# Optimization experiments

Hardware: AMD Instinct MI355X
Metric: run time of the kernel (lower is better)

## Reference

```python
import jax, jax.numpy as jnp
import numpy as np

LN_EPS = 1e-5
GRID_MIN, GRID_MAX = -1.0, 1.0


def make_grid(grid_size: int, spline_order: int) -> jnp.ndarray:
    h = (GRID_MAX - GRID_MIN) / grid_size
    # extended knot vector: grid_size + 2*spline_order + 1 knots
    return (jnp.arange(-spline_order, grid_size + spline_order + 1, dtype=jnp.float32) * h
            + GRID_MIN)


def b_splines(x: jnp.ndarray, grid: jnp.ndarray, k: int) -> jnp.ndarray:
    """Cox-de Boor B-spline bases. x: [B, in] -> [B, in, grid_size + k]."""
    x = x[..., None]  # [B, in, 1]
    bases = ((x >= grid[:-1]) & (x < grid[1:])).astype(x.dtype)
    for p in range(1, k + 1):
        left = (x - grid[: -(p + 1)]) / (grid[p:-1] - grid[: -(p + 1)]) * bases[..., :-1]
        right = (grid[p + 1:] - x) / (grid[p + 1:] - grid[1:-p]) * bases[..., 1:]
        bases = left + right
    return bases  # [B, in, grid_size + k]


def kan_layer(x, base_w, spline_w, grid, k):
    # base path: silu(x) @ base_w.T ; spline path: einsum over basis functions
    base = jnp.einsum('bi,oi->bo', jax.nn.silu(x), base_w)
    spl = jnp.einsum('big,oig->bo', b_splines(x, grid, k), spline_w)
    return base + spl


def layer_norm(x, gamma, beta):
    mu = jnp.mean(x, axis=-1, keepdims=True)
    var = jnp.mean(jnp.square(x - mu), axis=-1, keepdims=True)
    return (x - mu) * jax.lax.rsqrt(var + LN_EPS) * gamma + beta


def setup_inputs() -> dict:
    key = jax.random.key(0)
    ks = jax.random.split(key, 6)
    B, S, H, A = 32768, 256, 512, 64
    G, K = 5, 3
    nb = G + K  # 8 basis functions per edge
    s = 0.1
    return {
        'state': jax.random.normal(ks[0], (B, S), dtype=jnp.float32),
        'feat_base_w': jax.random.normal(ks[1], (H, S), dtype=jnp.float32) * s,
        'feat_spline_w': jax.random.normal(ks[2], (H, S, nb), dtype=jnp.float32) * s,
        'ln_gamma': jnp.ones((H,), dtype=jnp.float32),
        'ln_beta': jnp.zeros((H,), dtype=jnp.float32),
        'mean_base_w': jax.random.normal(ks[3], (A, H), dtype=jnp.float32) * s,
        'mean_spline_w': jax.random.normal(ks[4], (A, H, nb), dtype=jnp.float32) * s,
        'lstd_base_w': jax.random.normal(ks[5], (A, H), dtype=jnp.float32) * s,
        'lstd_spline_w': jax.random.normal(jax.random.fold_in(key, 7), (A, H, nb), dtype=jnp.float32) * s,
        'grid_size': G,
        'spline_order': K,
    }


def reference(state, feat_base_w, feat_spline_w, ln_gamma, ln_beta,
              mean_base_w, mean_spline_w, lstd_base_w, lstd_spline_w,
              grid_size, spline_order):
    LOG_STD_MIN, LOG_STD_MAX = -20.0, 2.0
    grid = make_grid(grid_size, spline_order)
    x = kan_layer(state, feat_base_w, feat_spline_w, grid, spline_order)
    x = jax.nn.relu(layer_norm(x, ln_gamma, ln_beta))
    mean = jnp.tanh(kan_layer(x, mean_base_w, mean_spline_w, grid, spline_order))
    log_std = jnp.clip(kan_layer(x, lstd_base_w, lstd_spline_w, grid, spline_order),
                       LOG_STD_MIN, LOG_STD_MAX)
    return mean, log_std
```

## Files before the change

### kernel.cpp

```cpp
#include <hip/hip_runtime.h>
#include <stdint.h>

typedef __bf16 bf16x8 __attribute__((ext_vector_type(8)));
typedef float f32x4 __attribute__((ext_vector_type(4)));
typedef unsigned short u16x8 __attribute__((ext_vector_type(8)));
typedef unsigned int as1_uint __attribute__((address_space(1)));
typedef unsigned int as3_uint __attribute__((address_space(3)));

#define N_B 32768
#define S_IN 256
#define H_DIM 512
#define A_DIM 64
#define K1_DIM 2304
#define K2_DIM 4608
#define LDA2 72

#define MFMA __builtin_amdgcn_mfma_f32_16x16x32_bf16

static __device__ __forceinline__ unsigned short f2bf(float f) {
  union { float f; unsigned u; } v; v.f = f;
  unsigned r = v.u + 0x7fffu + ((v.u >> 16) & 1u);
  return (unsigned short)(r >> 16);
}

static __device__ __forceinline__ void gload_lds16(const void* g, void* l) {
  __builtin_amdgcn_global_load_lds((const as1_uint*)g, (as3_uint*)l, 16, 0, 0);
}

static __device__ __forceinline__ int swz64(int c, int row) {
  return (c & ~63) | ((((c >> 3) & 7) ^ (row & 7)) << 3) | (c & 7);
}

static __device__ __forceinline__ void bspline_w(float x, float& c,
    float& w0, float& w1, float& w2, float& w3) {
  float u = fmaf(2.5f, x, 5.5f);
  c = floorf(u);
  float f = u - c;
  float f2 = f * f;
  float f3 = f2 * f;
  const float k6 = 1.f / 6.f;
  w3 = f3 * k6;
  w2 = (3.f * (f + f2 - f3) + 1.f) * k6;
  w1 = (3.f * f3 - 6.f * f2 + 4.f) * k6;
  float omf = 1.f - f;
  w0 = omf * omf * omf * k6;
}

static __device__ __forceinline__ float silu_f(float x) {
  return x / (1.f + __expf(-x));
}

__global__ void k_sentinel(float* out, int n) {
  int i = blockIdx.x * blockDim.x + threadIdx.x;
  for (; i < n; i += gridDim.x * blockDim.x) out[i] = 12345.f;
}

__global__ void k_prep_w1(const float* __restrict__ base_w,
                          const float* __restrict__ spline_w,
                          unsigned short* __restrict__ W1) {
  int idx = blockIdx.x * blockDim.x + threadIdx.x;
  int n = idx / K1_DIM;
  int c = idx - n * K1_DIM;
  int k = swz64(c, n);
  int j = k >> 8;
  int i = k & 255;
  float v = (j == 0) ? base_w[n * S_IN + i]
                     : spline_w[(size_t)(n * S_IN + i) * 8 + (j - 1)];
  W1[idx] = f2bf(v);
}

__global__ void k_prep_w2(const float* __restrict__ mean_base,
                          const float* __restrict__ mean_spl,
                          const float* __restrict__ lstd_base,
                          const float* __restrict__ lstd_spl,
                          unsigned short* __restrict__ W2) {
  int idx = blockIdx.x * blockDim.x + threadIdx.x;
  int n = idx / K2_DIM;
  int c = idx - n * K2_DIM;
  int k = swz64(c, n);
  int j = k / 512;
  int h = k - j * 512;
  const float* bw = (n < 64) ? mean_base : lstd_base;
  const float* sw = (n < 64) ? mean_spl : lstd_spl;
  int nn = n & 63;
  float v = (j == 0) ? bw[nn * H_DIM + h]
                     : sw[(size_t)(nn * H_DIM + h) * 8 + (j - 1)];
  W2[idx] = f2bf(v);
}

__global__ void k_features1(const float* __restrict__ state,
                            unsigned short* __restrict__ F1) {
  int tid = blockIdx.x * blockDim.x + threadIdx.x;
  int base = tid * 4;
  int b = base >> 8;
  int i = base & 255;
  const float4 xv = *(const float4*)(state + base);
  float xs[4] = {xv.x, xv.y, xv.z, xv.w};
  unsigned short outj[9][4];
  #pragma unroll
  for (int e = 0; e < 4; ++e) {
    float x = xs[e];
    float c, w0, w1, w2, w3;
    bspline_w(x, c, w0, w1, w2, w3);
    outj[0][e] = f2bf(silu_f(x));
    #pragma unroll
    for (int g = 0; g < 8; ++g) {
      float d = c - (float)g;
      float v = 0.f;
      v = (d == 0.f) ? w3 : v;
      v = (d == 1.f) ? w2 : v;
      v = (d == 2.f) ? w1 : v;
      v = (d == 3.f) ? w0 : v;
      outj[g + 1][e] = f2bf(v);
    }
  }
  size_t rowbase = (size_t)b * K1_DIM;
  #pragma unroll
  for (int j = 0; j < 9; ++j) {
    int c = swz64(j * S_IN + i, b);
    *(ushort4*)(F1 + rowbase + c) =
        make_ushort4(outj[j][0], outj[j][1], outj[j][2], outj[j][3]);
  }
}

__global__ __launch_bounds__(256, 2) void k_gemm1(
    const unsigned short* __restrict__ F1,
    const unsigned short* __restrict__ W1,
    float* __restrict__ X) {
  extern __shared__ unsigned short smem[];
  unsigned short* As0 = smem;
  unsigned short* As1 = smem + 8192;
  unsigned short* Bs0 = smem + 16384;
  unsigned short* Bs1 = smem + 24576;

  const int t = threadIdx.x;
  const int bid = (int)(blockIdx.x & 7) * 128 + ((int)blockIdx.x >> 3);
  const int bm = bid >> 2;
  const int bn = bid & 3;

  const unsigned short* Ab = F1 + (size_t)bm * 128 * K1_DIM;
  const unsigned short* Bb = W1 + (size_t)bn * 128 * K1_DIM;

  const int srow = t >> 3;
  const int scol = (t & 7) * 8;

  auto stage = [&](int buf, int kt) {
    unsigned short* Ad = buf ? As1 : As0;
    unsigned short* Bd = buf ? Bs1 : Bs0;
    const size_t k0 = (size_t)kt * 64;
    #pragma unroll
    for (int q = 0; q < 4; ++q) {
      const int r = q * 32 + srow;
      gload_lds16(Ab + (size_t)r * K1_DIM + k0 + scol, Ad + r * 64 + scol);
      gload_lds16(Bb + (size_t)r * K1_DIM + k0 + scol, Bd + r * 64 + scol);
    }
  };

  const int wave = t >> 6;
  const int lane = t & 63;
  const int wm = (wave >> 1) * 64;
  const int wn = (wave & 1) * 64;
  const int lr = lane & 15;
  const int l4 = lane >> 4;

  f32x4 acc[4][4];
  #pragma unroll
  for (int i = 0; i < 4; ++i)
    #pragma unroll
    for (int jj = 0; jj < 4; ++jj)
      acc[i][jj] = (f32x4){0.f, 0.f, 0.f, 0.f};

  stage(0, 0);
  __syncthreads();
  int cur = 0;
  const int NT = K1_DIM / 64;
  for (int kt = 0; kt < NT; ++kt) {
    if (kt + 1 < NT) stage(cur ^ 1, kt + 1);
    const unsigned short* A0 = cur ? As1 : As0;
    const unsigned short* B0 = cur ? Bs1 : Bs0;
    #pragma unroll
    for (int ks = 0; ks < 2; ++ks) {
      bf16x8 af[4], bfv[4];
      #pragma unroll
      for (int fm = 0; fm < 4; ++fm) {
        const int r = wm + fm * 16 + lr;
        const int slot = (ks * 4 + l4) ^ (r & 7);
        af[fm] = *(const bf16x8*)(A0 + r * 64 + slot * 8);
      }
      #pragma unroll
      for (int fn = 0; fn < 4; ++fn) {
        const int r = wn + fn * 16 + lr;
        const int slot = (ks * 4 + l4) ^ (r & 7);
        bfv[fn] = *(const bf16x8*)(B0 + r * 64 + slot * 8);
      }
      #pragma unroll
      for (int fm = 0; fm < 4; ++fm)
        #pragma unroll
        for (int fn = 0; fn < 4; ++fn)
          acc[fm][fn] = MFMA(af[fm], bfv[fn], acc[fm][fn], 0, 0, 0);
    }
    __syncthreads();
    cur ^= 1;
  }

  float* Xb = X + (size_t)bm * 128 * H_DIM + bn * 128;
  #pragma unroll
  for (int fm = 0; fm < 4; ++fm) {
    const int row0 = wm + fm * 16 + l4 * 4;
    #pragma unroll
    for (int fn = 0; fn < 4; ++fn) {
      const int col = wn + fn * 16 + lr;
      #pragma unroll
      for (int r = 0; r < 4; ++r)
        Xb[(size_t)(row0 + r) * H_DIM + col] = acc[fm][fn][r];
    }
  }
}

__global__ __launch_bounds__(256, 2) void k_gemm2(
    const float* __restrict__ X, const unsigned short* __restrict__ W2,
    const float* __restrict__ gamma, const float* __restrict__ beta,
    float* __restrict__ out) {
  extern __shared__ unsigned short smem2[];
  unsigned short* At = smem2;
  unsigned short* Bt = smem2 + 64 * LDA2;

  const int t = threadIdx.x;
  const int bm = blockIdx.x;
  const int row = t >> 2;
  const int quart = t & 3;
  const int wave = t >> 6;
  const int lane = t & 63;
  const int wn = wave * 32;
  const int lr = lane & 15;
  const int l4 = lane >> 4;

  const float* Xrow = X + (size_t)(bm * 64 + row) * H_DIM;

  float s = 0.f, ss = 0.f;
  #pragma unroll 4
  for (int q = 0; q < 32; ++q) {
    float4 v = *(const float4*)(Xrow + quart * 128 + q * 4);
    s += v.x + v.y + v.z + v.w;
    ss += v.x * v.x + v.y * v.y + v.z * v.z + v.w * v.w;
  }
  s += __shfl_xor(s, 1); ss += __shfl_xor(ss, 1);
  s += __shfl_xor(s, 2); ss += __shfl_xor(ss, 2);
  const float mu = s * (1.f / 512.f);
  const float var = ss * (1.f / 512.f) - mu * mu;
  const float rstd = rsqrtf(var + 1e-5f);

  f32x4 acc[4][2];
  #pragma unroll
  for (int i = 0; i < 4; ++i)
    #pragma unroll
    for (int jj = 0; jj < 2; ++jj)
      acc[i][jj] = (f32x4){0.f, 0.f, 0.f, 0.f};

  float cw[16], w0[16], w1[16], w2[16], w3[16];

  const int sbrow = t >> 3;
  const int sbcol = (t & 7) * 8;

  for (int hb = 0; hb < 8; ++hb) {
    for (int j = 0; j < 9; ++j) {
      __syncthreads();
      {
        const size_t k0 = (size_t)j * 512 + hb * 64;
        #pragma unroll
        for (int q = 0; q < 4; ++q) {
          const int r = q * 32 + sbrow;
          gload_lds16(W2 + (size_t)r * K2_DIM + k0 + sbcol, Bt + r * 64 + sbcol);
        }
      }
      unsigned short av[16];
      if (j == 0) {
        #pragma unroll
        for (int c4 = 0; c4 < 4; ++c4) {
          const int h = hb * 64 + quart * 16 + c4 * 4;
          const float4 xv = *(const float4*)(Xrow + h);
          const float4 gv = *(const float4*)(gamma + h);
          const float4 bv = *(const float4*)(beta + h);
          float xa[4] = {xv.x, xv.y, xv.z, xv.w};
          float ga[4] = {gv.x, gv.y, gv.z, gv.w};
          float ba[4] = {bv.x, bv.y, bv.z, bv.w};
          #pragma unroll
          for (int e2 = 0; e2 < 4; ++e2) {
            const int e = c4 * 4 + e2;
            float xn = fmaf((xa[e2] - mu) * rstd, ga[e2], ba[e2]);
            xn = fmaxf(xn, 0.f);
            bspline_w(xn, cw[e], w0[e], w1[e], w2[e], w3[e]);
            av[e] = f2bf(silu_f(xn));
          }
        }
      } else {
        const float g = (float)(j - 1);
        #pragma unroll
        for (int e = 0; e < 16; ++e) {
          const float d = cw[e] - g;
          float v = 0.f;
          v = (d == 0.f) ? w3[e] : v;
          v = (d == 1.f) ? w2[e] : v;
          v = (d == 2.f) ? w1[e] : v;
          v = (d == 3.f) ? w0[e] : v;
          av[e] = f2bf(v);
        }
      }
      u16x8 p0, p1;
      #pragma unroll
      for (int e = 0; e < 8; ++e) { p0[e] = av[e]; p1[e] = av[e + 8]; }
      *(u16x8*)(At + row * LDA2 + quart * 16) = p0;
      *(u16x8*)(At + row * LDA2 + quart * 16 + 8) = p1;

      __syncthreads();

      #pragma unroll
      for (int ks = 0; ks < 2; ++ks) {
        bf16x8 af[4], bfv[2];
        #pragma unroll
        for (int fm = 0; fm < 4; ++fm)
          af[fm] = *(const bf16x8*)(At + (fm * 16 + lr) * LDA2 + ks * 32 + l4 * 8);
        #pragma unroll
        for (int fn = 0; fn < 2; ++fn) {
          const int r = wn + fn * 16 + lr;
          const int slot = (ks * 4 + l4) ^ (r & 7);
          bfv[fn] = *(const bf16x8*)(Bt + r * 64 + slot * 8);
        }
        #pragma unroll
        for (int fm = 0; fm < 4; ++fm)
          #pragma unroll
          for (int fn = 0; fn < 2; ++fn)
            acc[fm][fn] = MFMA(af[fm], bfv[fn], acc[fm][fn], 0, 0, 0);
      }
    }
  }

  float* mean_out = out;
  float* lstd_out = out + (size_t)N_B * A_DIM;
  #pragma unroll
  for (int fm = 0; fm < 4; ++fm) {
    const int r0 = bm * 64 + fm * 16 + l4 * 4;
    #pragma unroll
    for (int fn = 0; fn < 2; ++fn) {
      const int n = wn + fn * 16 + lr;
      #pragma unroll
      for (int r = 0; r < 4; ++r) {
        const float v = acc[fm][fn][r];
        if (n < 64) mean_out[(size_t)(r0 + r) * 64 + n] = tanhf(v);
        else lstd_out[(size_t)(r0 + r) * 64 + (n - 64)] = fminf(fmaxf(v, -20.f), 2.f);
      }
    }
  }
}

extern "C" void kernel_launch(void* const* d_in, const int* in_sizes, int n_in,
                              void* d_out, int out_size, void* d_ws, size_t ws_size,
                              hipStream_t stream) {
  const float* state         = (const float*)d_in[0];
  const float* feat_base_w   = (const float*)d_in[1];
  const float* feat_spline_w = (const float*)d_in[2];
  const float* ln_gamma      = (const float*)d_in[3];
  const float* ln_beta       = (const float*)d_in[4];
  const float* mean_base_w   = (const float*)d_in[5];
  const float* mean_spline_w = (const float*)d_in[6];
  const float* lstd_base_w   = (const float*)d_in[7];
  const float* lstd_spline_w = (const float*)d_in[8];

  const size_t W1_OFF = 0;
  const size_t W2_OFF = 2359296;
  const size_t F1_OFF = 3538944;
  const size_t X_OFF  = 154533888;
  const size_t NEED   = 221642752;

  if (ws_size < NEED) {
    hipLaunchKernelGGL(k_sentinel, dim3(4096), dim3(256), 0, stream,
                       (float*)d_out, out_size);
    return;
  }

  char* ws = (char*)d_ws;
  unsigned short* W1 = (unsigned short*)(ws + W1_OFF);
  unsigned short* W2 = (unsigned short*)(ws + W2_OFF);
  unsigned short* F1 = (unsigned short*)(ws + F1_OFF);
  float* X = (float*)(ws + X_OFF);

  hipLaunchKernelGGL(k_prep_w1, dim3(4608), dim3(256), 0, stream,
                     feat_base_w, feat_spline_w, W1);
  hipLaunchKernelGGL(k_prep_w2, dim3(2304), dim3(256), 0, stream,
                     mean_base_w, mean_spline_w, lstd_base_w, lstd_spline_w, W2);
  hipLaunchKernelGGL(k_features1, dim3(8192), dim3(256), 0, stream, state, F1);
  hipLaunchKernelGGL(k_gemm1, dim3(1024), dim3(256), 65536, stream, F1, W1, X);
  hipLaunchKernelGGL(k_gemm2, dim3(512), dim3(256), (64 * LDA2 + 128 * 64) * 2,
                     stream, X, W2, ln_gamma, ln_beta, (float*)d_out);
}
```

Measured before the change: 233.6 us.

## Interleave per-channel KAN features in gemm2 and load B fragments from global directly

Rearranges the second-layer weight matrix so that each hidden channel's base and 8 spline weights are interleaved and padded to 12 entries. The gemm2 A-tile is then built two channels per thread by packing silu and four nonzero B-spline weights with 64-bit shifts, instead of computing dense one-hot bases across 9 separate K-slices. B fragments are register-prefetched from global memory instead of staged through LDS, and the W2 buffer now reuses the F1 workspace after gemm1, so its prep runs later. The padding adds about a third more MFMA work and makes B loads uncoalesced global reads, in exchange for fewer barriers and less feature computation.

```diff
diff --git a/kernel.cpp b/kernel.cpp
--- a/kernel.cpp
+++ b/kernel.cpp
@@ -12,8 +12,8 @@
 #define H_DIM 512
 #define A_DIM 64
 #define K1_DIM 2304
-#define K2_DIM 4608
-#define LDA2 72
+#define K2P 6144
+#define LDA2P 104
 
 #define MFMA __builtin_amdgcn_mfma_f32_16x16x32_bf16
 
@@ -50,6 +50,37 @@
   return x / (1.f + __expf(-x));
 }
 
+static __device__ __forceinline__ void kan_feat(float x, unsigned& s16,
+    unsigned& q0, unsigned& q1, unsigned& q2, unsigned& q3) {
+  s16 = f2bf(silu_f(x));
+  float u = fmaf(2.5f, x, 5.5f);
+  float cf = floorf(u);
+  float f = u - cf;
+  float f2 = f * f;
+  float f3 = f2 * f;
+  const float k6 = 1.f / 6.f;
+  float w3v = f3 * k6;
+  float w2v = (3.f * (f + f2 - f3) + 1.f) * k6;
+  float w1v = (3.f * f3 - 6.f * f2 + 4.f) * k6;
+  float omf = 1.f - f;
+  float w0v = omf * omf * omf * k6;
+  int i0 = (int)cf - 3;
+  uint64_t W64 = (uint64_t)((unsigned)f2bf(w0v) | ((unsigned)f2bf(w1v) << 16))
+               | ((uint64_t)((unsigned)f2bf(w2v) | ((unsigned)f2bf(w3v) << 16)) << 32);
+  uint64_t lo = 0, hi = 0;
+  if (i0 >= 0) {
+    int s = i0 * 16;
+    lo = (i0 < 4) ? (W64 << (s & 63)) : 0;
+    uint64_t hr = (i0 >= 1 && i0 < 4) ? (W64 >> ((64 - s) & 63)) : 0;
+    uint64_t hl = (i0 >= 4 && i0 < 8) ? (W64 << ((s - 64) & 63)) : 0;
+    hi = hr | hl;
+  } else {
+    lo = (i0 >= -3) ? (W64 >> ((-i0 * 16) & 63)) : 0;
+  }
+  q0 = (unsigned)lo; q1 = (unsigned)(lo >> 32);
+  q2 = (unsigned)hi; q3 = (unsigned)(hi >> 32);
+}
+
 __global__ void k_sentinel(float* out, int n) {
   int i = blockIdx.x * blockDim.x + threadIdx.x;
   for (; i < n; i += gridDim.x * blockDim.x) out[i] = 12345.f;
@@ -73,19 +104,19 @@
                           const float* __restrict__ mean_spl,
                           const float* __restrict__ lstd_base,
                           const float* __restrict__ lstd_spl,
-                          unsigned short* __restrict__ W2) {
+                          unsigned short* __restrict__ W2p) {
   int idx = blockIdx.x * blockDim.x + threadIdx.x;
-  int n = idx / K2_DIM;
-  int c = idx - n * K2_DIM;
-  int k = swz64(c, n);
-  int j = k / 512;
-  int h = k - j * 512;
+  int n = idx / K2P;
+  int k = idx - n * K2P;
+  int h = k / 12;
+  int j = k - h * 12;
   const float* bw = (n < 64) ? mean_base : lstd_base;
   const float* sw = (n < 64) ? mean_spl : lstd_spl;
   int nn = n & 63;
-  float v = (j == 0) ? bw[nn * H_DIM + h]
-                     : sw[(size_t)(nn * H_DIM + h) * 8 + (j - 1)];
-  W2[idx] = f2bf(v);
+  float v = 0.f;
+  if (j == 0) v = bw[nn * H_DIM + h];
+  else if (j <= 8) v = sw[(size_t)(nn * H_DIM + h) * 8 + (j - 1)];
+  W2p[idx] = f2bf(v);
 }
 
 __global__ void k_features1(const float* __restrict__ state,
@@ -218,12 +249,11 @@
 }
 
 __global__ __launch_bounds__(256, 2) void k_gemm2(
-    const float* __restrict__ X, const unsigned short* __restrict__ W2,
+    const float* __restrict__ X, const unsigned short* __restrict__ W2p,
     const float* __restrict__ gamma, const float* __restrict__ beta,
     float* __restrict__ out) {
   extern __shared__ unsigned short smem2[];
   unsigned short* At = smem2;
-  unsigned short* Bt = smem2 + 64 * LDA2;
 
   const int t = threadIdx.x;
   const int bm = blockIdx.x;
@@ -250,6 +280,21 @@
   const float var = ss * (1.f / 512.f) - mu * mu;
   const float rstd = rsqrtf(var + 1e-5f);
 
+  const unsigned short* bptr0 = W2p + (size_t)(wn + lr) * K2P + l4 * 8;
+  const unsigned short* bptr1 = W2p + (size_t)(wn + 16 + lr) * K2P + l4 * 8;
+
+  bf16x8 bcur[2][3], bnxt[2][3];
+  #pragma unroll
+  for (int ks = 0; ks < 3; ++ks) {
+    bnxt[0][ks] = *(const bf16x8*)(bptr0 + ks * 32);
+    bnxt[1][ks] = *(const bf16x8*)(bptr1 + ks * 32);
+  }
+
+  const int hq = quart * 2;
+  float2 xp = *(const float2*)(Xrow + hq);
+  float2 gp = *(const float2*)(gamma + hq);
+  float2 bp = *(const float2*)(beta + hq);
+
   f32x4 acc[4][2];
   #pragma unroll
   for (int i = 0; i < 4; ++i)
@@ -257,80 +302,56 @@
     for (int jj = 0; jj < 2; ++jj)
       acc[i][jj] = (f32x4){0.f, 0.f, 0.f, 0.f};
 
-  float cw[16], w0[16], w1[16], w2[16], w3[16];
-
-  const int sbrow = t >> 3;
-  const int sbcol = (t & 7) * 8;
-
-  for (int hb = 0; hb < 8; ++hb) {
-    for (int j = 0; j < 9; ++j) {
-      __syncthreads();
-      {
-        const size_t k0 = (size_t)j * 512 + hb * 64;
-        #pragma unroll
-        for (int q = 0; q < 4; ++q) {
-          const int r = q * 32 + sbrow;
-          gload_lds16(W2 + (size_t)r * K2_DIM + k0 + sbcol, Bt + r * 64 + sbcol);
-        }
+  for (int ch = 0; ch < 64; ++ch) {
+    unsigned o[12];
+    {
+      float xn0 = fmaxf(fmaf((xp.x - mu) * rstd, gp.x, bp.x), 0.f);
+      float xn1 = fmaxf(fmaf((xp.y - mu) * rstd, gp.y, bp.y), 0.f);
+      unsigned sA, a0, a1, a2, a3, sB, b0, b1, b2, b3;
+      kan_feat(xn0, sA, a0, a1, a2, a3);
+      kan_feat(xn1, sB, b0, b1, b2, b3);
+      o[0] = sA | (a0 << 16); o[1] = (a0 >> 16) | (a1 << 16);
+      o[2] = (a1 >> 16) | (a2 << 16); o[3] = (a2 >> 16) | (a3 << 16);
+      o[4] = (a3 >> 16); o[5] = 0u;
+      o[6] = sB | (b0 << 16); o[7] = (b0 >> 16) | (b1 << 16);
+      o[8] = (b1 >> 16) | (b2 << 16); o[9] = (b2 >> 16) | (b3 << 16);
+      o[10] = (b3 >> 16); o[11] = 0u;
+    }
+    __syncthreads();
+    #pragma unroll
+    for (int fn = 0; fn < 2; ++fn)
+      #pragma unroll
+      for (int ks = 0; ks < 3; ++ks)
+        bcur[fn][ks] = bnxt[fn][ks];
+    {
+      uint4* da = (uint4*)(At + row * LDA2P + quart * 24);
+      da[0] = make_uint4(o[0], o[1], o[2], o[3]);
+      da[1] = make_uint4(o[4], o[5], o[6], o[7]);
+      da[2] = make_uint4(o[8], o[9], o[10], o[11]);
+    }
+    __syncthreads();
+    if (ch < 63) {
+      const int h2 = (ch + 1) * 8 + hq;
+      xp = *(const float2*)(Xrow + h2);
+      gp = *(const float2*)(gamma + h2);
+      bp = *(const float2*)(beta + h2);
+      const size_t ko = (size_t)(ch + 1) * 96;
+      #pragma unroll
+      for (int ks = 0; ks < 3; ++ks) {
+        bnxt[0][ks] = *(const bf16x8*)(bptr0 + ko + ks * 32);
+        bnxt[1][ks] = *(const bf16x8*)(bptr1 + ko + ks * 32);
       }
-      unsigned short av[16];
-      if (j == 0) {
-        #pragma unroll
-        for (int c4 = 0; c4 < 4; ++c4) {
-          const int h = hb * 64 + quart * 16 + c4 * 4;
-          const float4 xv = *(const float4*)(Xrow + h);
-          const float4 gv = *(const float4*)(gamma + h);
-          const float4 bv = *(const float4*)(beta + h);
-          float xa[4] = {xv.x, xv.y, xv.z, xv.w};
-          float ga[4] = {gv.x, gv.y, gv.z, gv.w};
-          float ba[4] = {bv.x, bv.y, bv.z, bv.w};
-          #pragma unroll
-          for (int e2 = 0; e2 < 4; ++e2) {
-            const int e = c4 * 4 + e2;
-            float xn = fmaf((xa[e2] - mu) * rstd, ga[e2], ba[e2]);
-            xn = fmaxf(xn, 0.f);
-            bspline_w(xn, cw[e], w0[e], w1[e], w2[e], w3[e]);
-            av[e] = f2bf(silu_f(xn));
-          }
-        }
-      } else {
-        const float g = (float)(j - 1);
-        #pragma unroll
-        for (int e = 0; e < 16; ++e) {
-          const float d = cw[e] - g;
-          float v = 0.f;
-          v = (d == 0.f) ? w3[e] : v;
-          v = (d == 1.f) ? w2[e] : v;
-          v = (d == 2.f) ? w1[e] : v;
-          v = (d == 3.f) ? w0[e] : v;
-          av[e] = f2bf(v);
-        }
-      }
-      u16x8 p0, p1;
-      #pragma unroll
-      for (int e = 0; e < 8; ++e) { p0[e] = av[e]; p1[e] = av[e + 8]; }
-      *(u16x8*)(At + row * LDA2 + quart * 16) = p0;
-      *(u16x8*)(At + row * LDA2 + quart * 16 + 8) = p1;
-
-      __syncthreads();
-
-      #pragma unroll
-      for (int ks = 0; ks < 2; ++ks) {
-        bf16x8 af[4], bfv[2];
-        #pragma unroll
-        for (int fm = 0; fm < 4; ++fm)
-          af[fm] = *(const bf16x8*)(At + (fm * 16 + lr) * LDA2 + ks * 32 + l4 * 8);
-        #pragma unroll
-        for (int fn = 0; fn < 2; ++fn) {
-          const int r = wn + fn * 16 + lr;
-          const int slot = (ks * 4 + l4) ^ (r & 7);
-          bfv[fn] = *(const bf16x8*)(Bt + r * 64 + slot * 8);
-        }
-        #pragma unroll
-        for (int fm = 0; fm < 4; ++fm)
-          #pragma unroll
-          for (int fn = 0; fn < 2; ++fn)
-            acc[fm][fn] = MFMA(af[fm], bfv[fn], acc[fm][fn], 0, 0, 0);
+    }
+    #pragma unroll
+    for (int ks = 0; ks < 3; ++ks) {
+      bf16x8 af[4];
+      #pragma unroll
+      for (int fm = 0; fm < 4; ++fm)
+        af[fm] = *(const bf16x8*)(At + (fm * 16 + lr) * LDA2P + ks * 32 + l4 * 8);
+      #pragma unroll
+      for (int fm = 0; fm < 4; ++fm) {
+        acc[fm][0] = MFMA(af[fm], bcur[0][ks], acc[fm][0], 0, 0, 0);
+        acc[fm][1] = MFMA(af[fm], bcur[1][ks], acc[fm][1], 0, 0, 0);
       }
     }
   }
@@ -366,11 +387,11 @@
   const float* lstd_base_w   = (const float*)d_in[7];
   const float* lstd_spline_w = (const float*)d_in[8];
 
-  const size_t W1_OFF = 0;
-  const size_t W2_OFF = 2359296;
-  const size_t F1_OFF = 3538944;
-  const size_t X_OFF  = 154533888;
-  const size_t NEED   = 221642752;
+  const size_t W1_OFF  = 0;
+  const size_t F1_OFF  = 2359296;
+  const size_t W2P_OFF = F1_OFF;
+  const size_t X_OFF   = 153354240;
+  const size_t NEED    = 220463104;
 
   if (ws_size < NEED) {
     hipLaunchKernelGGL(k_sentinel, dim3(4096), dim3(256), 0, stream,
@@ -379,17 +400,17 @@
   }
 
   char* ws = (char*)d_ws;
-  unsigned short* W1 = (unsigned short*)(ws + W1_OFF);
-  unsigned short* W2 = (unsigned short*)(ws + W2_OFF);
-  unsigned short* F1 = (unsigned short*)(ws + F1_OFF);
+  unsigned short* W1  = (unsigned short*)(ws + W1_OFF);
+  unsigned short* F1  = (unsigned short*)(ws + F1_OFF);
+  unsigned short* W2p = (unsigned short*)(ws + W2P_OFF);
   float* X = (float*)(ws + X_OFF);
 
   hipLaunchKernelGGL(k_prep_w1, dim3(4608), dim3(256), 0, stream,
                      feat_base_w, feat_spline_w, W1);
-  hipLaunchKernelGGL(k_prep_w2, dim3(2304), dim3(256), 0, stream,
-                     mean_base_w, mean_spline_w, lstd_base_w, lstd_spline_w, W2);
   hipLaunchKernelGGL(k_features1, dim3(8192), dim3(256), 0, stream, state, F1);
   hipLaunchKernelGGL(k_gemm1, dim3(1024), dim3(256), 65536, stream, F1, W1, X);
-  hipLaunchKernelGGL(k_gemm2, dim3(512), dim3(256), (64 * LDA2 + 128 * 64) * 2,
-                     stream, X, W2, ln_gamma, ln_beta, (float*)d_out);
-}
+  hipLaunchKernelGGL(k_prep_w2, dim3(3072), dim3(256), 0, stream,
+                     mean_base_w, mean_spline_w, lstd_base_w, lstd_spline_w, W2p);
+  hipLaunchKernelGGL(k_gemm2, dim3(512), dim3(256), 64 * LDA2P * 2, stream,
+                     X, W2p, ln_gamma, ln_beta, (float*)d_out);
+}
```

After: 246.5 us. +5.5%, slower.
